# Performance work log

Measured on AMD Instinct MI355X. Metric: run time of the kernel, lower is better.

Reference implementation:

```python
import jax, jax.numpy as jnp
import numpy as np
import math

B, S, E, H = 2, 2048, 1024, 16
D = E // H  # head_dim = 64


def setup_inputs() -> dict:
    key = jax.random.key(0)
    ks = jax.random.split(key, 5)
    scale_p = 1.0 / math.sqrt(D)
    return {
        "x": jax.random.normal(ks[0], (B, S, E), dtype=jnp.float32),
        "Wq": jax.random.normal(ks[1], (D, D), dtype=jnp.float32) * scale_p,
        "Wk": jax.random.normal(ks[2], (D, D), dtype=jnp.float32) * scale_p,
        "Wv": jax.random.normal(ks[3], (D, D), dtype=jnp.float32) * scale_p,
        "W_out": jax.random.normal(ks[4], (E, E), dtype=jnp.float32) * (1.0 / math.sqrt(E)),
        "b_out": jnp.zeros((E,), dtype=jnp.float32),
    }


def reference(x, Wq, Wk, Wv, W_out, b_out):
    b, s, e = x.shape
    xh = x.reshape(b, s, H, D)  # [B,S,H,D]
    # per-head linear projections (torch Linear: y = x @ W.T), weights shared across heads
    q = jnp.einsum("bshd,ed->bshe", xh, Wq)
    k = jnp.einsum("bshd,ed->bshe", xh, Wk)
    v = jnp.einsum("bshd,ed->bshe", xh, Wv)
    # scaled dot-product attention, scale = sqrt(embed_dim) per tutorial-style impl
    energy = jnp.einsum("bqhd,bkhd->bhqk", q, k) / jnp.sqrt(jnp.float32(e))
    attn = jax.nn.softmax(energy, axis=-1)  # [B,H,S,S]
    out = jnp.einsum("bhqk,bkhd->bqhd", attn, v).reshape(b, s, e)
    return out @ W_out.T + b_out
```

## Files before the change

### kernel.cpp

```cpp
#include <hip/hip_runtime.h>
#include <math.h>

#define BB 2
#define SS 2048
#define EE 1024
#define HH 16
#define DD 64
constexpr int NROWS = BB * SS * HH;
constexpr float SCALE_Q = 1.4426950408889634f / 32.0f;

typedef __attribute__((ext_vector_type(8))) short bf16x8;
typedef __attribute__((ext_vector_type(4))) float f32x4;
typedef __attribute__((ext_vector_type(16))) float f32x16;
typedef __attribute__((ext_vector_type(4))) unsigned u32x4;

__device__ inline unsigned cvt_pk(float lo, float hi) {
  unsigned r;
  asm("v_cvt_pk_bf16_f32 %0, %1, %2" : "=v"(r) : "v"(lo), "v"(hi));
  return r;
}

__global__ __launch_bounds__(256) void qkv_mfma(
    const float* __restrict__ x,
    const float* __restrict__ Wq, const float* __restrict__ Wk,
    const float* __restrict__ Wv, const float* __restrict__ Wo,
    ushort* __restrict__ qo, ushort* __restrict__ ko, ushort* __restrict__ vto,
    ushort* __restrict__ wob) {
  __shared__ __align__(16) ushort Xs[64 * 72];
  __shared__ __align__(16) ushort Ws[3][64 * 72];
  const int tid = threadIdx.x, w = tid >> 6, l = tid & 63;
  const int g = l >> 4, c = l & 15;
  const int s0 = blockIdx.x * 64, h = blockIdx.y, b = blockIdx.z;

  {
    const int lin = blockIdx.x + (blockIdx.y << 5) + (blockIdx.z << 9);
    const size_t base = (size_t)lin * 1024 + tid * 4;
    float4 a = *(const float4*)&Wo[base];
    uint2 r;
    r.x = cvt_pk(a.x, a.y);
    r.y = cvt_pk(a.z, a.w);
    *(uint2*)&wob[base] = r;
  }

  for (int i = tid; i < 1536; i += 256) {
    int t = i >> 9, j = i & 511;
    int r = j >> 3, e0 = (j & 7) * 8;
    const float* W = (t == 0) ? Wq : ((t == 1) ? Wk : Wv);
    float4 va = *(const float4*)&W[r * 64 + e0];
    float4 vb = *(const float4*)&W[r * 64 + e0 + 4];
    u32x4 pk;
    pk[0] = cvt_pk(va.x, va.y);
    pk[1] = cvt_pk(va.z, va.w);
    pk[2] = cvt_pk(vb.x, vb.y);
    pk[3] = cvt_pk(vb.z, vb.w);
    *(u32x4*)&Ws[t][r * 72 + e0] = pk;
  }
  for (int i = tid; i < 1024; i += 256) {
    int r = i >> 4, c4 = (i & 15) * 4;
    float4 xv = *(const float4*)&x[(((size_t)b * SS + s0 + r) * HH + h) * DD + c4];
    uint2 pk;
    pk.x = cvt_pk(xv.x, xv.y);
    pk.y = cvt_pk(xv.z, xv.w);
    *(uint2*)&Xs[r * 72 + c4] = pk;
  }
  __syncthreads();

  bf16x8 a0 = *(bf16x8*)&Xs[(w * 16 + c) * 72 + g * 8];
  bf16x8 a1 = *(bf16x8*)&Xs[(w * 16 + c) * 72 + 32 + g * 8];

#pragma unroll
  for (int t = 0; t < 2; ++t) {
    ushort* out = (t == 0) ? qo : ko;
    const float sc = (t == 0) ? SCALE_Q : 1.0f;
#pragma unroll
    for (int ct = 0; ct < 4; ++ct) {
      bf16x8 b0 = *(bf16x8*)&Ws[t][(ct * 16 + c) * 72 + g * 8];
      bf16x8 b1 = *(bf16x8*)&Ws[t][(ct * 16 + c) * 72 + 32 + g * 8];
      f32x4 acc = (f32x4){0.f, 0.f, 0.f, 0.f};
      acc = __builtin_amdgcn_mfma_f32_16x16x32_bf16(b0, a0, acc, 0, 0, 0);
      acc = __builtin_amdgcn_mfma_f32_16x16x32_bf16(b1, a1, acc, 0, 0, 0);
      uint2 pk;
      pk.x = cvt_pk(acc[0] * sc, acc[1] * sc);
      pk.y = cvt_pk(acc[2] * sc, acc[3] * sc);
      int srow = s0 + w * 16 + c;
      *(uint2*)&out[((size_t)b * SS + srow) * EE + h * DD + ct * 16 + g * 4] = pk;
    }
  }
#pragma unroll
  for (int ct = 0; ct < 4; ++ct) {
    bf16x8 b0 = *(bf16x8*)&Ws[2][(ct * 16 + c) * 72 + g * 8];
    bf16x8 b1 = *(bf16x8*)&Ws[2][(ct * 16 + c) * 72 + 32 + g * 8];
    f32x4 acc = (f32x4){0.f, 0.f, 0.f, 0.f};
    acc = __builtin_amdgcn_mfma_f32_16x16x32_bf16(a0, b0, acc, 0, 0, 0);
    acc = __builtin_amdgcn_mfma_f32_16x16x32_bf16(a1, b1, acc, 0, 0, 0);
    uint2 pk;
    pk.x = cvt_pk(acc[0], acc[1]);
    pk.y = cvt_pk(acc[2], acc[3]);
    int d = ct * 16 + c;
    int srow = w * 16 + g * 4;
    *(uint2*)&vto[(((size_t)b * HH + h) * DD + d) * SS + s0 + srow] = pk;
  }
}

__global__ __launch_bounds__(256) void attn_mfma(
    const ushort* __restrict__ q, const ushort* __restrict__ k,
    const ushort* __restrict__ vt, ushort* __restrict__ o) {
  __shared__ __align__(16) ushort Ks[2][64 * 72];
  __shared__ __align__(16) ushort Vts[2][64 * 72];
  const int tid = threadIdx.x, w = tid >> 6, l = tid & 63;
  const int lq = l & 31, h2 = l >> 5;
  const int work = ((blockIdx.x & 7) << 6) | (blockIdx.x >> 3);
  const int qt = work & 15, hb = work >> 4;
  const int h = hb & 15, b = hb >> 4;
  const int q0 = qt * 128 + w * 32;

  const size_t bh_qk = (size_t)b * SS * EE + h * DD;
  const size_t bh_vt = (size_t)b * SS * EE + h * (DD * SS);

  const int sr0 = tid >> 3;
  const int se0 = (tid & 7) * 8;
  const int krow0 = (sr0 & 19) | ((sr0 & 4) << 1) | ((sr0 & 8) >> 1);

  {
    bf16x8 kr0 = *(const bf16x8*)&k[bh_qk + (size_t)sr0 * EE + se0];
    bf16x8 kr1 = *(const bf16x8*)&k[bh_qk + (size_t)(sr0 + 32) * EE + se0];
    bf16x8 vr0 = *(const bf16x8*)&vt[bh_vt + (size_t)sr0 * SS + se0];
    bf16x8 vr1 = *(const bf16x8*)&vt[bh_vt + (size_t)(sr0 + 32) * SS + se0];
    *(bf16x8*)&Ks[0][krow0 * 72 + se0] = kr0;
    *(bf16x8*)&Ks[0][(krow0 + 32) * 72 + se0] = kr1;
    *(bf16x8*)&Vts[0][sr0 * 72 + se0] = vr0;
    *(bf16x8*)&Vts[0][(sr0 + 32) * 72 + se0] = vr1;
  }

  bf16x8 aq[4];
#pragma unroll
  for (int db = 0; db < 4; ++db)
    aq[db] = *(const bf16x8*)&q[bh_qk + (size_t)(q0 + lq) * EE + db * 16 + h2 * 8];

  f32x16 accO[2];
  float lacc[2] = {0.f, 0.f};
#pragma unroll
  for (int ct = 0; ct < 2; ++ct)
#pragma unroll
    for (int r = 0; r < 16; ++r) accO[ct][r] = 0.f;

  u32x4 pwvP[2][2];
  bf16x8 vfP[2][4];

  __syncthreads();

  {
    bf16x8 kr0 = *(const bf16x8*)&k[bh_qk + (size_t)(64 + sr0) * EE + se0];
    bf16x8 kr1 = *(const bf16x8*)&k[bh_qk + (size_t)(64 + sr0 + 32) * EE + se0];
    bf16x8 vr0 = *(const bf16x8*)&vt[bh_vt + 64 + (size_t)sr0 * SS + se0];
    bf16x8 vr1 = *(const bf16x8*)&vt[bh_vt + 64 + (size_t)(sr0 + 32) * SS + se0];

    f32x16 s[2];
#pragma unroll
    for (int kb = 0; kb < 2; ++kb) {
      f32x16 acc;
#pragma unroll
      for (int r = 0; r < 16; ++r) acc[r] = 0.f;
#pragma unroll
      for (int db = 0; db < 4; ++db) {
        bf16x8 ka = *(bf16x8*)&Ks[0][(kb * 32 + lq) * 72 + db * 16 + h2 * 8];
        acc = __builtin_amdgcn_mfma_f32_32x32x16_bf16(ka, aq[db], acc, 0, 0, 0);
      }
      s[kb] = acc;
    }
#pragma unroll
    for (int kb = 0; kb < 2; ++kb)
#pragma unroll
      for (int t16 = 0; t16 < 2; ++t16)
#pragma unroll
        for (int j2 = 0; j2 < 4; ++j2) {
          float pa = __builtin_amdgcn_exp2f(s[kb][t16 * 8 + j2 * 2]);
          float pb = __builtin_amdgcn_exp2f(s[kb][t16 * 8 + j2 * 2 + 1]);
          lacc[kb] += pa + pb;
          pwvP[kb][t16][j2] = cvt_pk(pa, pb);
        }
#pragma unroll
    for (int ct = 0; ct < 2; ++ct)
#pragma unroll
      for (int kb = 0; kb < 2; ++kb)
#pragma unroll
        for (int t16 = 0; t16 < 2; ++t16)
          vfP[ct][kb * 2 + t16] = *(bf16x8*)&Vts[0][(ct * 32 + lq) * 72 +
                                                    kb * 32 + t16 * 16 + h2 * 8];
    *(bf16x8*)&Ks[1][krow0 * 72 + se0] = kr0;
    *(bf16x8*)&Ks[1][(krow0 + 32) * 72 + se0] = kr1;
    *(bf16x8*)&Vts[1][sr0 * 72 + se0] = vr0;
    *(bf16x8*)&Vts[1][(sr0 + 32) * 72 + se0] = vr1;
    __syncthreads();
  }

  for (int t = 1; t < 32; ++t) {
    const int cur = t & 1;
    const int tn = (t + 1) & 31;

    bf16x8 kr0, kr1, vr0, vr1;
    {
      const size_t kb2 = bh_qk + (size_t)(tn * 64) * EE;
      kr0 = *(const bf16x8*)&k[kb2 + (size_t)sr0 * EE + se0];
      kr1 = *(const bf16x8*)&k[kb2 + (size_t)(sr0 + 32) * EE + se0];
      const size_t vb2 = bh_vt + tn * 64;
      vr0 = *(const bf16x8*)&vt[vb2 + (size_t)sr0 * SS + se0];
      vr1 = *(const bf16x8*)&vt[vb2 + (size_t)(sr0 + 32) * SS + se0];
    }

#pragma unroll
    for (int ct = 0; ct < 2; ++ct)
#pragma unroll
      for (int kb = 0; kb < 2; ++kb)
#pragma unroll
        for (int t16 = 0; t16 < 2; ++t16)
          accO[ct] = __builtin_amdgcn_mfma_f32_32x32x16_bf16(
              vfP[ct][kb * 2 + t16],
              __builtin_bit_cast(bf16x8, pwvP[kb][t16]), accO[ct], 0, 0, 0);

    f32x16 s[2];
#pragma unroll
    for (int kb = 0; kb < 2; ++kb) {
      f32x16 acc;
#pragma unroll
      for (int r = 0; r < 16; ++r) acc[r] = 0.f;
#pragma unroll
      for (int db = 0; db < 4; ++db) {
        bf16x8 ka = *(bf16x8*)&Ks[cur][(kb * 32 + lq) * 72 + db * 16 + h2 * 8];
        acc = __builtin_amdgcn_mfma_f32_32x32x16_bf16(ka, aq[db], acc, 0, 0, 0);
      }
      s[kb] = acc;
    }

    u32x4 pwvC[2][2];
#pragma unroll
    for (int kb = 0; kb < 2; ++kb)
#pragma unroll
      for (int t16 = 0; t16 < 2; ++t16)
#pragma unroll
        for (int j2 = 0; j2 < 4; ++j2) {
          float pa = __builtin_amdgcn_exp2f(s[kb][t16 * 8 + j2 * 2]);
          float pb = __builtin_amdgcn_exp2f(s[kb][t16 * 8 + j2 * 2 + 1]);
          lacc[kb] += pa + pb;
          pwvC[kb][t16][j2] = cvt_pk(pa, pb);
        }

#pragma unroll
    for (int ct = 0; ct < 2; ++ct)
#pragma unroll
      for (int kb = 0; kb < 2; ++kb)
#pragma unroll
        for (int t16 = 0; t16 < 2; ++t16)
          vfP[ct][kb * 2 + t16] = *(bf16x8*)&Vts[cur][(ct * 32 + lq) * 72 +
                                                      kb * 32 + t16 * 16 + h2 * 8];

    {
      const int nxt = cur ^ 1;
      *(bf16x8*)&Ks[nxt][krow0 * 72 + se0] = kr0;
      *(bf16x8*)&Ks[nxt][(krow0 + 32) * 72 + se0] = kr1;
      *(bf16x8*)&Vts[nxt][sr0 * 72 + se0] = vr0;
      *(bf16x8*)&Vts[nxt][(sr0 + 32) * 72 + se0] = vr1;
    }
    __syncthreads();

#pragma unroll
    for (int kb = 0; kb < 2; ++kb)
#pragma unroll
      for (int t16 = 0; t16 < 2; ++t16) pwvP[kb][t16] = pwvC[kb][t16];
  }

#pragma unroll
  for (int ct = 0; ct < 2; ++ct)
#pragma unroll
    for (int kb = 0; kb < 2; ++kb)
#pragma unroll
      for (int t16 = 0; t16 < 2; ++t16)
        accO[ct] = __builtin_amdgcn_mfma_f32_32x32x16_bf16(
            vfP[ct][kb * 2 + t16],
            __builtin_bit_cast(bf16x8, pwvP[kb][t16]), accO[ct], 0, 0, 0);

  {
    float tsum = lacc[0] + lacc[1];
    tsum += __shfl_xor(tsum, 32, 64);
    float inv = 1.f / tsum;
    size_t row = (size_t)b * SS + q0 + lq;
#pragma unroll
    for (int ct = 0; ct < 2; ++ct)
#pragma unroll
      for (int rq = 0; rq < 4; ++rq) {
        uint2 pk;
        pk.x = cvt_pk(accO[ct][rq * 4 + 0] * inv, accO[ct][rq * 4 + 1] * inv);
        pk.y = cvt_pk(accO[ct][rq * 4 + 2] * inv, accO[ct][rq * 4 + 3] * inv);
        *(uint2*)&o[row * EE + h * DD + ct * 32 + rq * 8 + h2 * 4] = pk;
      }
  }
}

__global__ __launch_bounds__(256) void out_proj_mfma(
    const ushort* __restrict__ a, const ushort* __restrict__ wo,
    const float* __restrict__ bias, float* __restrict__ y) {
  __shared__ __align__(16) ushort As[2][128 * 72];
  __shared__ __align__(16) ushort Ws[2][128 * 72];
  const int tid = threadIdx.x, l = tid & 63;
  const int wv = tid >> 6, wm = wv >> 1, wn = wv & 1;
  const int lq = l & 31, h2 = l >> 5;
  const int m0 = blockIdx.x * 128, n0 = blockIdx.y * 128;
  const int sr = tid >> 3, se = (tid & 7) * 8;
  const int krow0 = (sr & 19) | ((sr & 4) << 1) | ((sr & 8) >> 1);

  f32x16 acc[2][2];
#pragma unroll
  for (int mb = 0; mb < 2; ++mb)
#pragma unroll
    for (int nb = 0; nb < 2; ++nb)
#pragma unroll
      for (int r = 0; r < 16; ++r) acc[mb][nb][r] = 0.f;

  {
#pragma unroll
    for (int j = 0; j < 4; ++j) {
      int r = sr + j * 32;
      *(bf16x8*)&As[0][r * 72 + se] = *(const bf16x8*)&a[(size_t)(m0 + r) * EE + se];
      *(bf16x8*)&Ws[0][(j * 32 + krow0) * 72 + se] =
          *(const bf16x8*)&wo[(size_t)(n0 + r) * EE + se];
    }
  }
  __syncthreads();

  for (int t = 0; t < 16; ++t) {
    const int cur = t & 1;
    bf16x8 Arg[4], Brg[4];
    if (t < 15) {
      const int k0 = (t + 1) * 64;
#pragma unroll
      for (int j = 0; j < 4; ++j) {
        int r = sr + j * 32;
        Arg[j] = *(const bf16x8*)&a[(size_t)(m0 + r) * EE + k0 + se];
        Brg[j] = *(const bf16x8*)&wo[(size_t)(n0 + r) * EE + k0 + se];
      }
    }

    bf16x8 af[2][4];
#pragma unroll
    for (int mb = 0; mb < 2; ++mb)
#pragma unroll
      for (int db = 0; db < 4; ++db)
        af[mb][db] = *(bf16x8*)&As[cur][(wm * 64 + mb * 32 + lq) * 72 +
                                        db * 16 + h2 * 8];
#pragma unroll
    for (int nb = 0; nb < 2; ++nb)
#pragma unroll
      for (int db = 0; db < 4; ++db) {
        bf16x8 wf = *(bf16x8*)&Ws[cur][(wn * 64 + nb * 32 + lq) * 72 +
                                       db * 16 + h2 * 8];
#pragma unroll
        for (int mb = 0; mb < 2; ++mb)
          acc[mb][nb] = __builtin_amdgcn_mfma_f32_32x32x16_bf16(
              wf, af[mb][db], acc[mb][nb], 0, 0, 0);
      }

    if (t < 15) {
      const int nxt = cur ^ 1;
#pragma unroll
      for (int j = 0; j < 4; ++j) {
        int r = sr + j * 32;
        *(bf16x8*)&As[nxt][r * 72 + se] = Arg[j];
        *(bf16x8*)&Ws[nxt][(j * 32 + krow0) * 72 + se] = Brg[j];
      }
    }
    __syncthreads();
  }

#pragma unroll
  for (int mb = 0; mb < 2; ++mb) {
    const size_t row = (size_t)(m0 + wm * 64 + mb * 32 + lq) * EE;
#pragma unroll
    for (int nb = 0; nb < 2; ++nb)
#pragma unroll
      for (int t16 = 0; t16 < 2; ++t16) {
        const int nbase = n0 + wn * 64 + nb * 32 + t16 * 16 + h2 * 8;
        float4 bv0 = *(const float4*)&bias[nbase];
        float4 bv1 = *(const float4*)&bias[nbase + 4];
        float4 o0 = {acc[mb][nb][t16 * 8 + 0] + bv0.x,
                     acc[mb][nb][t16 * 8 + 1] + bv0.y,
                     acc[mb][nb][t16 * 8 + 2] + bv0.z,
                     acc[mb][nb][t16 * 8 + 3] + bv0.w};
        float4 o1 = {acc[mb][nb][t16 * 8 + 4] + bv1.x,
                     acc[mb][nb][t16 * 8 + 5] + bv1.y,
                     acc[mb][nb][t16 * 8 + 6] + bv1.z,
                     acc[mb][nb][t16 * 8 + 7] + bv1.w};
        *(float4*)&y[row + nbase] = o0;
        *(float4*)&y[row + nbase + 4] = o1;
      }
  }
}

extern "C" void kernel_launch(void* const* d_in, const int* in_sizes, int n_in,
                              void* d_out, int out_size, void* d_ws,
                              size_t ws_size, hipStream_t stream) {
  const float* x = (const float*)d_in[0];
  const float* Wq = (const float*)d_in[1];
  const float* Wk = (const float*)d_in[2];
  const float* Wv = (const float*)d_in[3];
  const float* Wo = (const float*)d_in[4];
  const float* bo = (const float*)d_in[5];
  float* out = (float*)d_out;

  const size_t per = (size_t)NROWS * 64;
  ushort* qb = (ushort*)d_ws;
  ushort* kb = qb + per;
  ushort* vtb = kb + per;
  ushort* aob = vtb + per;
  ushort* wob = aob + per;

  qkv_mfma<<<dim3(32, 16, 2), 256, 0, stream>>>(x, Wq, Wk, Wv, Wo,
                                                qb, kb, vtb, wob);
  attn_mfma<<<512, 256, 0, stream>>>(qb, kb, vtb, aob);
  out_proj_mfma<<<dim3(32, 8), 256, 0, stream>>>(aob, wob, bo, out);
}
```

Before: 79.20 us.

## Deepen attention software pipeline so exp overlaps QK and PV MFMAs

Restructures the attention inner loop into a three-stage software pipeline: each iteration computes QK^T for tile t, exp for tile t-1, and PV for tile t-2, with an extra prologue and epilogue. The aim is to keep the exp/convert work on VALU independent of the MFMAs issued in the same iteration, so the scheduler can overlap transcendental work with matrix ops. In exchange it holds more live registers (an extra score tile and an extra set of V fragments), which may raise VGPR pressure and lower occupancy.

```diff
diff --git a/kernel.cpp b/kernel.cpp
--- a/kernel.cpp
+++ b/kernel.cpp
@@ -144,8 +144,59 @@
 #pragma unroll
     for (int r = 0; r < 16; ++r) accO[ct][r] = 0.f;
 
-  u32x4 pwvP[2][2];
-  bf16x8 vfP[2][4];
+  f32x16 sA[2];
+  u32x4 pwvA[2][2];
+  bf16x8 vfA[2][4];
+  bf16x8 vfB[2][4];
+
+  auto do_qk = [&](int cur, f32x16 (&sOut)[2]) {
+#pragma unroll
+    for (int kb = 0; kb < 2; ++kb) {
+      f32x16 acc;
+#pragma unroll
+      for (int r = 0; r < 16; ++r) acc[r] = 0.f;
+#pragma unroll
+      for (int db = 0; db < 4; ++db) {
+        bf16x8 ka = *(bf16x8*)&Ks[cur][(kb * 32 + lq) * 72 + db * 16 + h2 * 8];
+        acc = __builtin_amdgcn_mfma_f32_32x32x16_bf16(ka, aq[db], acc, 0, 0, 0);
+      }
+      sOut[kb] = acc;
+    }
+  };
+  auto do_exp = [&](const f32x16 (&sIn)[2], u32x4 (&pwvOut)[2][2]) {
+#pragma unroll
+    for (int kb = 0; kb < 2; ++kb)
+#pragma unroll
+      for (int t16 = 0; t16 < 2; ++t16)
+#pragma unroll
+        for (int j2 = 0; j2 < 4; ++j2) {
+          float pa = __builtin_amdgcn_exp2f(sIn[kb][t16 * 8 + j2 * 2]);
+          float pb = __builtin_amdgcn_exp2f(sIn[kb][t16 * 8 + j2 * 2 + 1]);
+          lacc[kb] += pa + pb;
+          pwvOut[kb][t16][j2] = cvt_pk(pa, pb);
+        }
+  };
+  auto do_pv = [&](const u32x4 (&pwv)[2][2], const bf16x8 (&vf)[2][4]) {
+#pragma unroll
+    for (int ct = 0; ct < 2; ++ct)
+#pragma unroll
+      for (int kb = 0; kb < 2; ++kb)
+#pragma unroll
+        for (int t16 = 0; t16 < 2; ++t16)
+          accO[ct] = __builtin_amdgcn_mfma_f32_32x32x16_bf16(
+              vf[ct][kb * 2 + t16],
+              __builtin_bit_cast(bf16x8, pwv[kb][t16]), accO[ct], 0, 0, 0);
+  };
+  auto do_capture = [&](int cur, bf16x8 (&vf)[2][4]) {
+#pragma unroll
+    for (int ct = 0; ct < 2; ++ct)
+#pragma unroll
+      for (int kb = 0; kb < 2; ++kb)
+#pragma unroll
+        for (int t16 = 0; t16 < 2; ++t16)
+          vf[ct][kb * 2 + t16] = *(bf16x8*)&Vts[cur][(ct * 32 + lq) * 72 +
+                                                     kb * 32 + t16 * 16 + h2 * 8];
+  };
 
   __syncthreads();
 
@@ -154,39 +205,8 @@
     bf16x8 kr1 = *(const bf16x8*)&k[bh_qk + (size_t)(64 + sr0 + 32) * EE + se0];
     bf16x8 vr0 = *(const bf16x8*)&vt[bh_vt + 64 + (size_t)sr0 * SS + se0];
     bf16x8 vr1 = *(const bf16x8*)&vt[bh_vt + 64 + (size_t)(sr0 + 32) * SS + se0];
-
-    f32x16 s[2];
-#pragma unroll
-    for (int kb = 0; kb < 2; ++kb) {
-      f32x16 acc;
-#pragma unroll
-      for (int r = 0; r < 16; ++r) acc[r] = 0.f;
-#pragma unroll
-      for (int db = 0; db < 4; ++db) {
-        bf16x8 ka = *(bf16x8*)&Ks[0][(kb * 32 + lq) * 72 + db * 16 + h2 * 8];
-        acc = __builtin_amdgcn_mfma_f32_32x32x16_bf16(ka, aq[db], acc, 0, 0, 0);
-      }
-      s[kb] = acc;
-    }
-#pragma unroll
-    for (int kb = 0; kb < 2; ++kb)
-#pragma unroll
-      for (int t16 = 0; t16 < 2; ++t16)
-#pragma unroll
-        for (int j2 = 0; j2 < 4; ++j2) {
-          float pa = __builtin_amdgcn_exp2f(s[kb][t16 * 8 + j2 * 2]);
-          float pb = __builtin_amdgcn_exp2f(s[kb][t16 * 8 + j2 * 2 + 1]);
-          lacc[kb] += pa + pb;
-          pwvP[kb][t16][j2] = cvt_pk(pa, pb);
-        }
-#pragma unroll
-    for (int ct = 0; ct < 2; ++ct)
-#pragma unroll
-      for (int kb = 0; kb < 2; ++kb)
-#pragma unroll
-        for (int t16 = 0; t16 < 2; ++t16)
-          vfP[ct][kb * 2 + t16] = *(bf16x8*)&Vts[0][(ct * 32 + lq) * 72 +
-                                                    kb * 32 + t16 * 16 + h2 * 8];
+    do_qk(0, sA);
+    do_capture(0, vfB);
     *(bf16x8*)&Ks[1][krow0 * 72 + se0] = kr0;
     *(bf16x8*)&Ks[1][(krow0 + 32) * 72 + se0] = kr1;
     *(bf16x8*)&Vts[1][sr0 * 72 + se0] = vr0;
@@ -194,7 +214,29 @@
     __syncthreads();
   }
 
-  for (int t = 1; t < 32; ++t) {
+  {
+    bf16x8 kr0 = *(const bf16x8*)&k[bh_qk + (size_t)(128 + sr0) * EE + se0];
+    bf16x8 kr1 = *(const bf16x8*)&k[bh_qk + (size_t)(128 + sr0 + 32) * EE + se0];
+    bf16x8 vr0 = *(const bf16x8*)&vt[bh_vt + 128 + (size_t)sr0 * SS + se0];
+    bf16x8 vr1 = *(const bf16x8*)&vt[bh_vt + 128 + (size_t)(sr0 + 32) * SS + se0];
+    do_exp(sA, pwvA);
+    f32x16 sN[2];
+    do_qk(1, sN);
+#pragma unroll
+    for (int ct = 0; ct < 2; ++ct)
+#pragma unroll
+      for (int j = 0; j < 4; ++j) vfA[ct][j] = vfB[ct][j];
+    do_capture(1, vfB);
+#pragma unroll
+    for (int kb = 0; kb < 2; ++kb) sA[kb] = sN[kb];
+    *(bf16x8*)&Ks[0][krow0 * 72 + se0] = kr0;
+    *(bf16x8*)&Ks[0][(krow0 + 32) * 72 + se0] = kr1;
+    *(bf16x8*)&Vts[0][sr0 * 72 + se0] = vr0;
+    *(bf16x8*)&Vts[0][(sr0 + 32) * 72 + se0] = vr1;
+    __syncthreads();
+  }
+
+  for (int t = 2; t < 32; ++t) {
     const int cur = t & 1;
     const int tn = (t + 1) & 31;
 
@@ -208,51 +250,23 @@
       vr1 = *(const bf16x8*)&vt[vb2 + (size_t)(sr0 + 32) * SS + se0];
     }
 
+    u32x4 pwvN[2][2];
+    do_exp(sA, pwvN);
+    do_pv(pwvA, vfA);
+    f32x16 sN[2];
+    do_qk(cur, sN);
+
 #pragma unroll
     for (int ct = 0; ct < 2; ++ct)
 #pragma unroll
-      for (int kb = 0; kb < 2; ++kb)
-#pragma unroll
-        for (int t16 = 0; t16 < 2; ++t16)
-          accO[ct] = __builtin_amdgcn_mfma_f32_32x32x16_bf16(
-              vfP[ct][kb * 2 + t16],
-              __builtin_bit_cast(bf16x8, pwvP[kb][t16]), accO[ct], 0, 0, 0);
-
-    f32x16 s[2];
+      for (int j = 0; j < 4; ++j) vfA[ct][j] = vfB[ct][j];
+    do_capture(cur, vfB);
 #pragma unroll
     for (int kb = 0; kb < 2; ++kb) {
-      f32x16 acc;
-#pragma unroll
-      for (int r = 0; r < 16; ++r) acc[r] = 0.f;
-#pragma unroll
-      for (int db = 0; db < 4; ++db) {
-        bf16x8 ka = *(bf16x8*)&Ks[cur][(kb * 32 + lq) * 72 + db * 16 + h2 * 8];
-        acc = __builtin_amdgcn_mfma_f32_32x32x16_bf16(ka, aq[db], acc, 0, 0, 0);
-      }
-      s[kb] = acc;
-    }
-
-    u32x4 pwvC[2][2];
-#pragma unroll
-    for (int kb = 0; kb < 2; ++kb)
-#pragma unroll
-      for (int t16 = 0; t16 < 2; ++t16)
-#pragma unroll
-        for (int j2 = 0; j2 < 4; ++j2) {
-          float pa = __builtin_amdgcn_exp2f(s[kb][t16 * 8 + j2 * 2]);
-          float pb = __builtin_amdgcn_exp2f(s[kb][t16 * 8 + j2 * 2 + 1]);
-          lacc[kb] += pa + pb;
-          pwvC[kb][t16][j2] = cvt_pk(pa, pb);
-        }
-
-#pragma unroll
-    for (int ct = 0; ct < 2; ++ct)
-#pragma unroll
-      for (int kb = 0; kb < 2; ++kb)
-#pragma unroll
-        for (int t16 = 0; t16 < 2; ++t16)
-          vfP[ct][kb * 2 + t16] = *(bf16x8*)&Vts[cur][(ct * 32 + lq) * 72 +
-                                                      kb * 32 + t16 * 16 + h2 * 8];
+      sA[kb] = sN[kb];
+#pragma unroll
+      for (int t16 = 0; t16 < 2; ++t16) pwvA[kb][t16] = pwvN[kb][t16];
+    }
 
     {
       const int nxt = cur ^ 1;
@@ -262,22 +276,14 @@
       *(bf16x8*)&Vts[nxt][(sr0 + 32) * 72 + se0] = vr1;
     }
     __syncthreads();
-
-#pragma unroll
-    for (int kb = 0; kb < 2; ++kb)
-#pragma unroll
-      for (int t16 = 0; t16 < 2; ++t16) pwvP[kb][t16] = pwvC[kb][t16];
-  }
-
-#pragma unroll
-  for (int ct = 0; ct < 2; ++ct)
-#pragma unroll
-    for (int kb = 0; kb < 2; ++kb)
-#pragma unroll
-      for (int t16 = 0; t16 < 2; ++t16)
-        accO[ct] = __builtin_amdgcn_mfma_f32_32x32x16_bf16(
-            vfP[ct][kb * 2 + t16],
-            __builtin_bit_cast(bf16x8, pwvP[kb][t16]), accO[ct], 0, 0, 0);
+  }
+
+  do_pv(pwvA, vfA);
+  {
+    u32x4 pwvN[2][2];
+    do_exp(sA, pwvN);
+    do_pv(pwvN, vfB);
+  }
 
   {
     float tsum = lacc[0] + lacc[1];
```

Measured after the change: 89.46 us. +13.0%, slower.

## Stage K/V tiles via direct global-to-LDS loads with XOR-swizzled layout

Applied to the files above, without the earlier changes.

Replaces the register-staged double-buffered K and V^T tile loads in the attention kernel with global_load_lds DMA writes straight into shared memory, issued one tile ahead. The padded 72-element LDS rows become unpadded 64-element rows, with an XOR chunk swizzle to avoid bank conflicts on the MFMA fragment reads. This removes the VGPRs and ds_write instructions that held prefetched tiles, and cuts LDS footprint. The cost is relying on the barrier correctly waiting for the async LDS loads, and on the swizzle and row permutation matching between writer and readers.

```diff
diff --git a/kernel.cpp b/kernel.cpp
--- a/kernel.cpp
+++ b/kernel.cpp
@@ -18,6 +18,12 @@
   unsigned r;
   asm("v_cvt_pk_bf16_f32 %0, %1, %2" : "=v"(r) : "v"(lo), "v"(hi));
   return r;
+}
+
+__device__ inline void gload_lds16(const ushort* src, ushort* ldsdst) {
+  __builtin_amdgcn_global_load_lds(
+      (const __attribute__((address_space(1))) void*)src,
+      (__attribute__((address_space(3))) void*)ldsdst, 16, 0, 0);
 }
 
 __global__ __launch_bounds__(256) void qkv_mfma(
@@ -105,8 +111,8 @@
 __global__ __launch_bounds__(256) void attn_mfma(
     const ushort* __restrict__ q, const ushort* __restrict__ k,
     const ushort* __restrict__ vt, ushort* __restrict__ o) {
-  __shared__ __align__(16) ushort Ks[2][64 * 72];
-  __shared__ __align__(16) ushort Vts[2][64 * 72];
+  __shared__ __align__(16) ushort Ks[2][64 * 64];
+  __shared__ __align__(16) ushort Vts[2][64 * 64];
   const int tid = threadIdx.x, w = tid >> 6, l = tid & 63;
   const int lq = l & 31, h2 = l >> 5;
   const int work = ((blockIdx.x & 7) << 6) | (blockIdx.x >> 3);
@@ -118,19 +124,23 @@
   const size_t bh_vt = (size_t)b * SS * EE + h * (DD * SS);
 
   const int sr0 = tid >> 3;
-  const int se0 = (tid & 7) * 8;
-  const int krow0 = (sr0 & 19) | ((sr0 & 4) << 1) | ((sr0 & 8) >> 1);
-
-  {
-    bf16x8 kr0 = *(const bf16x8*)&k[bh_qk + (size_t)sr0 * EE + se0];
-    bf16x8 kr1 = *(const bf16x8*)&k[bh_qk + (size_t)(sr0 + 32) * EE + se0];
-    bf16x8 vr0 = *(const bf16x8*)&vt[bh_vt + (size_t)sr0 * SS + se0];
-    bf16x8 vr1 = *(const bf16x8*)&vt[bh_vt + (size_t)(sr0 + 32) * SS + se0];
-    *(bf16x8*)&Ks[0][krow0 * 72 + se0] = kr0;
-    *(bf16x8*)&Ks[0][(krow0 + 32) * 72 + se0] = kr1;
-    *(bf16x8*)&Vts[0][sr0 * 72 + se0] = vr0;
-    *(bf16x8*)&Vts[0][(sr0 + 32) * 72 + se0] = vr1;
-  }
+  const int c7 = tid & 7;
+  const int ksrow = (sr0 & 19) | ((sr0 & 4) << 1) | ((sr0 & 8) >> 1);
+  const int schunk = (c7 ^ (sr0 & 7)) * 8;
+  const int ldsw = w * 512;
+
+  auto stage = [&](int buf, int tile) {
+    const size_t kbase = bh_qk + (size_t)(tile * 64) * EE;
+    const size_t vbase = bh_vt + tile * 64;
+    gload_lds16(&k[kbase + (size_t)ksrow * EE + schunk], &Ks[buf][ldsw]);
+    gload_lds16(&k[kbase + (size_t)(32 + ksrow) * EE + schunk],
+                &Ks[buf][2048 + ldsw]);
+    gload_lds16(&vt[vbase + (size_t)sr0 * SS + schunk], &Vts[buf][ldsw]);
+    gload_lds16(&vt[vbase + (size_t)(32 + sr0) * SS + schunk],
+                &Vts[buf][2048 + ldsw]);
+  };
+
+  stage(0, 0);
 
   bf16x8 aq[4];
 #pragma unroll
@@ -150,11 +160,7 @@
   __syncthreads();
 
   {
-    bf16x8 kr0 = *(const bf16x8*)&k[bh_qk + (size_t)(64 + sr0) * EE + se0];
-    bf16x8 kr1 = *(const bf16x8*)&k[bh_qk + (size_t)(64 + sr0 + 32) * EE + se0];
-    bf16x8 vr0 = *(const bf16x8*)&vt[bh_vt + 64 + (size_t)sr0 * SS + se0];
-    bf16x8 vr1 = *(const bf16x8*)&vt[bh_vt + 64 + (size_t)(sr0 + 32) * SS + se0];
-
+    stage(1, 1);
     f32x16 s[2];
 #pragma unroll
     for (int kb = 0; kb < 2; ++kb) {
@@ -163,7 +169,8 @@
       for (int r = 0; r < 16; ++r) acc[r] = 0.f;
 #pragma unroll
       for (int db = 0; db < 4; ++db) {
-        bf16x8 ka = *(bf16x8*)&Ks[0][(kb * 32 + lq) * 72 + db * 16 + h2 * 8];
+        bf16x8 ka = *(bf16x8*)&Ks[0][(kb * 32 + lq) * 64 +
+                                     (((db * 2 + h2) ^ (lq & 7)) * 8)];
         acc = __builtin_amdgcn_mfma_f32_32x32x16_bf16(ka, aq[db], acc, 0, 0, 0);
       }
       s[kb] = acc;
@@ -185,12 +192,9 @@
       for (int kb = 0; kb < 2; ++kb)
 #pragma unroll
         for (int t16 = 0; t16 < 2; ++t16)
-          vfP[ct][kb * 2 + t16] = *(bf16x8*)&Vts[0][(ct * 32 + lq) * 72 +
-                                                    kb * 32 + t16 * 16 + h2 * 8];
-    *(bf16x8*)&Ks[1][krow0 * 72 + se0] = kr0;
-    *(bf16x8*)&Ks[1][(krow0 + 32) * 72 + se0] = kr1;
-    *(bf16x8*)&Vts[1][sr0 * 72 + se0] = vr0;
-    *(bf16x8*)&Vts[1][(sr0 + 32) * 72 + se0] = vr1;
+          vfP[ct][kb * 2 + t16] =
+              *(bf16x8*)&Vts[0][(ct * 32 + lq) * 64 +
+                                (((kb * 4 + t16 * 2 + h2) ^ (lq & 7)) * 8)];
     __syncthreads();
   }
 
@@ -198,15 +202,7 @@
     const int cur = t & 1;
     const int tn = (t + 1) & 31;
 
-    bf16x8 kr0, kr1, vr0, vr1;
-    {
-      const size_t kb2 = bh_qk + (size_t)(tn * 64) * EE;
-      kr0 = *(const bf16x8*)&k[kb2 + (size_t)sr0 * EE + se0];
-      kr1 = *(const bf16x8*)&k[kb2 + (size_t)(sr0 + 32) * EE + se0];
-      const size_t vb2 = bh_vt + tn * 64;
-      vr0 = *(const bf16x8*)&vt[vb2 + (size_t)sr0 * SS + se0];
-      vr1 = *(const bf16x8*)&vt[vb2 + (size_t)(sr0 + 32) * SS + se0];
-    }
+    stage(cur ^ 1, tn);
 
 #pragma unroll
     for (int ct = 0; ct < 2; ++ct)
@@ -226,7 +222,8 @@
       for (int r = 0; r < 16; ++r) acc[r] = 0.f;
 #pragma unroll
       for (int db = 0; db < 4; ++db) {
-        bf16x8 ka = *(bf16x8*)&Ks[cur][(kb * 32 + lq) * 72 + db * 16 + h2 * 8];
+        bf16x8 ka = *(bf16x8*)&Ks[cur][(kb * 32 + lq) * 64 +
+                                       (((db * 2 + h2) ^ (lq & 7)) * 8)];
         acc = __builtin_amdgcn_mfma_f32_32x32x16_bf16(ka, aq[db], acc, 0, 0, 0);
       }
       s[kb] = acc;
@@ -251,16 +248,10 @@
       for (int kb = 0; kb < 2; ++kb)
 #pragma unroll
         for (int t16 = 0; t16 < 2; ++t16)
-          vfP[ct][kb * 2 + t16] = *(bf16x8*)&Vts[cur][(ct * 32 + lq) * 72 +
-                                                      kb * 32 + t16 * 16 + h2 * 8];
-
-    {
-      const int nxt = cur ^ 1;
-      *(bf16x8*)&Ks[nxt][krow0 * 72 + se0] = kr0;
-      *(bf16x8*)&Ks[nxt][(krow0 + 32) * 72 + se0] = kr1;
-      *(bf16x8*)&Vts[nxt][sr0 * 72 + se0] = vr0;
-      *(bf16x8*)&Vts[nxt][(sr0 + 32) * 72 + se0] = vr1;
-    }
+          vfP[ct][kb * 2 + t16] =
+              *(bf16x8*)&Vts[cur][(ct * 32 + lq) * 64 +
+                                  (((kb * 4 + t16 * 2 + h2) ^ (lq & 7)) * 8)];
+
     __syncthreads();
 
 #pragma unroll
```

New measurement: 87.07 us. +9.9%, slower.
